# Kernel tuning notes

Measured on AMD Instinct MI355X. Metric: run time of the kernel, lower is better.

Reference implementation:

```python
import jax, jax.numpy as jnp
import numpy as np

B, T, IN, H, L, OUT, PRED, FN = 512, 96, 64, 512, 2, 1, 24, 32


def setup_inputs() -> dict:
    key = jax.random.key(0)
    ks = jax.random.split(key, 12)
    sc = 0.02
    n = lambda i, shape: jax.random.normal(ks[i], shape, jnp.float32) * sc
    return {
        "x": jax.random.normal(ks[0], (B, T, IN), jnp.float32),
        "station_id": jax.random.randint(ks[1], (B,), 0, 26, jnp.int32),
        "W_hidden": n(2, (H, IN)), "b_hidden": jnp.zeros((H,), jnp.float32),
        "embed": n(3, (26, H)),
        "W_ih": n(4, (L, 4 * H, H)), "W_hh": n(5, (L, 4 * H, H)),
        "b_ih": jnp.zeros((L, 4 * H), jnp.float32), "b_hh": jnp.zeros((L, 4 * H), jnp.float32),
        "conv_W": n(6, (FN, T - 1)), "conv_b": jnp.zeros((FN,), jnp.float32),
        "W1": n(7, (FN, H)), "b1": jnp.zeros((FN,), jnp.float32),
        "W2": n(8, (H, H + FN)), "b2": jnp.zeros((H,), jnp.float32),
        "W_out": n(9, (T * OUT, H)), "b_out": jnp.zeros((T * OUT,), jnp.float32),
    }


def _lstm(xc, W_ih, W_hh, b_ih, b_hh):
    # xc: [B, T, H]; multi-layer LSTM, PyTorch gate order i,f,g,o
    n_layers = W_ih.shape[0]
    h0 = jnp.zeros((n_layers, xc.shape[0], W_hh.shape[-1]), xc.dtype)

    def step(carry, xt):
        h, c = carry  # [L, B, H]
        inp = xt
        hs, cs = [], []
        for l in range(n_layers):
            g = inp @ W_ih[l].T + h[l] @ W_hh[l].T + b_ih[l] + b_hh[l]
            i, f, gg, o = jnp.split(g, 4, axis=-1)
            cn = jax.nn.sigmoid(f) * c[l] + jax.nn.sigmoid(i) * jnp.tanh(gg)
            hn = jax.nn.sigmoid(o) * jnp.tanh(cn)
            hs.append(hn); cs.append(cn)
            inp = hn
        return (jnp.stack(hs), jnp.stack(cs)), inp  # emit last-layer h

    _, outs = jax.lax.scan(step, (h0, h0), jnp.swapaxes(xc, 0, 1))
    return jnp.swapaxes(outs, 0, 1)  # [B, T, H] last-layer hidden states


def reference(x, station_id, W_hidden, b_hidden, embed, W_ih, W_hh, b_ih, b_hh,
              conv_W, conv_b, W1, b1, W2, b2, W_out, b_out):
    b, t, _ = x.shape
    hdim = W_hidden.shape[0]
    fn = conv_W.shape[0]
    xc = jax.nn.relu(x @ W_hidden.T + b_hidden)
    xc = xc + embed[station_id][:, None, :]
    hs_seq = _lstm(xc, W_ih, W_hh, b_ih, b_hh)          # [B, T, H]
    Hmat = jax.nn.relu(hs_seq[:, :-1, :])                # [B, T-1, H]
    htt = hs_seq[:, -1, :]                               # [B, H]
    # Conv2d(1, FN, (T-1, 1)) over [B,1,T-1,H] == contraction over time
    conv = jax.nn.relu(jnp.einsum('bth,ft->bfh', Hmat, conv_W) + conv_b[None, :, None])
    # original does .view(-1, feat_size, filter_num): raw reshape, not transpose
    feat = conv.reshape(b, hdim, fn)                     # [B, H, FN]
    w = (htt @ W1.T + b1)[:, None, :]                    # [B, 1, FN]
    alpha = jax.nn.sigmoid(jnp.sum(feat * w, axis=2))    # [B, H]
    v = jnp.sum(alpha[:, :, None] * feat, axis=1)        # [B, FN]
    new_ht = jnp.concatenate([htt, v], axis=1) @ W2.T + b2
    ypred = (new_ht @ W_out.T + b_out)[:, -PRED * OUT:]
    return ypred
```

## Files before the change

### kernel.cpp

```cpp
#include <hip/hip_runtime.h>
#include <math.h>

namespace {

constexpr int B = 512, T = 96, IN = 64, H = 512, G4 = 2048;
constexpr int FN = 32, KC = 544, NPRED = 24, TM1 = T - 1;
constexpr int BH = B * H;

typedef __attribute__((ext_vector_type(8))) short s8v;
typedef __attribute__((ext_vector_type(16))) float f16v;

__device__ __forceinline__ float sigf(float x) { return 1.0f / (1.0f + __expf(-x)); }
__device__ __forceinline__ float tanhfast(float x) {
  x = fminf(fmaxf(x, -15.f), 15.f);
  float e = __expf(2.0f * x);
  return (e - 1.0f) / (e + 1.0f);
}
__device__ __forceinline__ unsigned short bf16_rne(float f) {
  unsigned u = __float_as_uint(f);
  u += 0x7fffu + ((u >> 16) & 1u);
  return (unsigned short)(u >> 16);
}
__device__ __forceinline__ void split8(const float4& x, const float4& y, s8v& hi, s8v& lo) {
  float vs[8] = {x.x, x.y, x.z, x.w, y.x, y.y, y.z, y.w};
#pragma unroll
  for (int j = 0; j < 8; ++j) {
    unsigned ub = __float_as_uint(vs[j]);
    hi[j] = (short)(ub >> 16);
    lo[j] = (short)bf16_rne(vs[j] - __uint_as_float(ub & 0xffff0000u));
  }
}

__global__ __launch_bounds__(256) void k_xc(
    const float* __restrict__ x, const int* __restrict__ sid,
    const float* __restrict__ Wh, const float* __restrict__ bh,
    const float* __restrict__ emb, float* __restrict__ planes) {
  constexpr int RWS = 64;
  int row0 = blockIdx.x * RWS;
  int tid = threadIdx.x;
  __shared__ __align__(16) float sx[RWS][IN];
  {
    const float4* xsrc = (const float4*)(x + (size_t)row0 * IN);
    float4* sdst = (float4*)(&sx[0][0]);
    for (int i = tid; i < RWS * IN / 4; i += 256) sdst[i] = xsrc[i];
  }
  float4 w0[16], w1[16];
  const float* wr0 = Wh + (size_t)tid * IN;
  const float* wr1 = Wh + (size_t)(tid + 256) * IN;
#pragma unroll
  for (int j = 0; j < 16; ++j) {
    w0[j] = *(const float4*)(wr0 + j * 4);
    w1[j] = *(const float4*)(wr1 + j * 4);
  }
  float bb0 = bh[tid], bb1 = bh[tid + 256];
  __syncthreads();
#pragma unroll 2
  for (int r = 0; r < RWS; ++r) {
    float a00 = bb0, a01 = 0.f, a02 = 0.f, a03 = 0.f;
    float a10 = bb1, a11 = 0.f, a12 = 0.f, a13 = 0.f;
#pragma unroll
    for (int j = 0; j < 16; ++j) {
      float4 xv = *(const float4*)(&sx[r][j * 4]);
      a00 = fmaf(xv.x, w0[j].x, a00);
      a01 = fmaf(xv.y, w0[j].y, a01);
      a02 = fmaf(xv.z, w0[j].z, a02);
      a03 = fmaf(xv.w, w0[j].w, a03);
      a10 = fmaf(xv.x, w1[j].x, a10);
      a11 = fmaf(xv.y, w1[j].y, a11);
      a12 = fmaf(xv.z, w1[j].z, a12);
      a13 = fmaf(xv.w, w1[j].w, a13);
    }
    float acc0 = (a00 + a01) + (a02 + a03);
    float acc1 = (a10 + a11) + (a12 + a13);
    int row = row0 + r;
    int bb = row / T, t = row % T;
    const float* eb = emb + (size_t)sid[bb] * H;
    size_t o = ((size_t)t * B + bb) * H;
    planes[o + tid] = fmaxf(acc0, 0.f) + eb[tid];
    planes[o + tid + 256] = fmaxf(acc1, 0.f) + eb[tid + 256];
  }
}

__global__ __launch_bounds__(256) void k_wswz(
    const float* __restrict__ Wih, const float* __restrict__ Whh,
    short* __restrict__ WFhi, short* __restrict__ WFlo) {
  int g = blockIdx.x * 256 + threadIdx.x;
  int lane = g & 63;
  int fi = g >> 6;
  int nt = fi & 3, kt = (fi >> 2) & 63, ng = (fi >> 8) & 15, layer = fi >> 12;
  int row = nt * H + ng * 32 + (lane & 31);
  int kk = kt * 16 + (lane >> 5) * 8;
  const float* src = (kk < H) ? (Wih + ((size_t)layer * G4 + row) * H + kk)
                              : (Whh + ((size_t)layer * G4 + row) * H + (kk - H));
  float4 f0 = *(const float4*)src, f1 = *(const float4*)(src + 4);
  s8v hi, lo;
  split8(f0, f1, hi, lo);
  size_t o = (size_t)fi * 512 + lane * 8;
  *(s8v*)(WFhi + o) = hi;
  *(s8v*)(WFlo + o) = lo;
}

__global__ __launch_bounds__(256) void k_w2t(
    const float* __restrict__ W2, float* __restrict__ W2T4) {
  int g = blockIdx.x * 256 + threadIdx.x;
  int h = g / KC, k = g % KC;
  W2T4[((size_t)(k >> 2) * H + h) * 4 + (k & 3)] = W2[g];
}

__global__ __launch_bounds__(256, 1) void k_step(
    int tt, float* __restrict__ planes, const short* __restrict__ WFhi,
    const short* __restrict__ WFlo, short* __restrict__ hFhi,
    short* __restrict__ hFlo, const float* __restrict__ bih,
    const float* __restrict__ bhh, float* __restrict__ c0,
    float* __restrict__ c1) {
  int gid = blockIdx.x;
  int xcd = gid & 7;
  int u = gid >> 3;
  int combo = xcd * 4 + (u & 3);
  int layer = combo >> 4;
  if (layer ? (tt == 0) : (tt == T)) return;
  int ng = combo & 15;
  int b0 = (u >> 2) * 64;
  int step = layer ? (tt - 1) : tt;
  int tid = threadIdx.x, lane = tid & 63, wk = tid >> 6;
  int l31 = lane & 31, lh = lane >> 5;

  __shared__ float comb[4][4][32][32];

  const float* bi = bih + (size_t)layer * G4;
  const float* bh2 = bhh + (size_t)layer * G4;
  float* cbuf = layer ? c1 : c0;

  int rpar = (step - 1) & 1;
  const float* xbase = nullptr;
  const short *abhi = nullptr, *ablo = nullptr;
  if (layer == 0 && wk < 2) {
    xbase = planes + (size_t)step * BH + (size_t)(b0 + l31) * H + wk * 256 + lh * 8;
  } else {
    int src = (layer == 0) ? 0 : ((wk < 2) ? 0 : 1);
    int par = (layer == 0) ? rpar : ((wk < 2) ? (step & 1) : rpar);
    int kk0 = wk * 16 - ((layer == 0 || wk >= 2) ? 32 : 0);
    size_t o = ((((size_t)src * 2 + par) * 32 + kk0) * H + (b0 + l31)) * 16 + lh * 8;
    abhi = hFhi + o;
    ablo = hFlo + o;
  }

  float bias[4];
#pragma unroll
  for (int nt = 0; nt < 4; ++nt) {
    int r = nt * H + ng * 32 + l31;
    bias[nt] = bi[r] + bh2[r];
  }

  const size_t wstep = 4 * 512;
  const size_t wbase0 = ((size_t)(layer * 16 + ng) * 64 + wk * 16) * wstep + (size_t)lane * 8;
  const size_t astep = (size_t)H * 16;

  f16v acc[2][4];
#pragma unroll
  for (int rt = 0; rt < 2; ++rt)
#pragma unroll
    for (int nt = 0; nt < 4; ++nt)
#pragma unroll
      for (int e = 0; e < 16; ++e) acc[rt][nt][e] = 0.f;

  s8v a0h0, a0l0, a0h1, a0l1, b0h0, b0h1, b0h2, b0h3, b0l0, b0l1, b0l2, b0l3;
  s8v a1h0, a1l0, a1h1, a1l1, b1h0, b1h1, b1h2, b1h3, b1l0, b1l1, b1l2, b1l3;
  s8v a2h0, a2l0, a2h1, a2l1, b2h0, b2h1, b2h2, b2h3, b2l0, b2l1, b2l2, b2l3;

#define LOADW_(kq, bh0, bh1, bh2, bh3, bl0, bl1, bl2, bl3)          \
  {                                                                 \
    size_t wo = wbase0 + (size_t)(kq) * wstep;                      \
    bh0 = *(const s8v*)(WFhi + wo);                                 \
    bh1 = *(const s8v*)(WFhi + wo + 512);                           \
    bh2 = *(const s8v*)(WFhi + wo + 1024);                          \
    bh3 = *(const s8v*)(WFhi + wo + 1536);                          \
    bl0 = *(const s8v*)(WFlo + wo);                                 \
    bl1 = *(const s8v*)(WFlo + wo + 512);                           \
    bl2 = *(const s8v*)(WFlo + wo + 1024);                          \
    bl3 = *(const s8v*)(WFlo + wo + 1536);                          \
  }
#define LOADA_(kq, ah0, al0, ah1, al1)                              \
  {                                                                 \
    if (xbase) {                                                    \
      const float* ap = xbase + (kq) * 16;                          \
      float4 f0 = *(const float4*)ap, f1 = *(const float4*)(ap + 4);\
      split8(f0, f1, ah0, al0);                                     \
      const float* aq = ap + 32 * H;                                \
      float4 g0 = *(const float4*)aq, g1 = *(const float4*)(aq + 4);\
      split8(g0, g1, ah1, al1);                                     \
    } else {                                                        \
      const short* ph_ = abhi + (size_t)(kq) * astep;               \
      const short* pl_ = ablo + (size_t)(kq) * astep;               \
      ah0 = *(const s8v*)(ph_);                                     \
      al0 = *(const s8v*)(pl_);                                     \
      ah1 = *(const s8v*)(ph_ + 512);                               \
      al1 = *(const s8v*)(pl_ + 512);                               \
    }                                                               \
  }
#define MFMA3R_(rt, ah, al, bh0, bh1, bh2, bh3, bl0, bl1, bl2, bl3)                        \
  {                                                                                        \
    acc[rt][0] = __builtin_amdgcn_mfma_f32_32x32x16_bf16(ah, bh0, acc[rt][0], 0, 0, 0);    \
    acc[rt][1] = __builtin_amdgcn_mfma_f32_32x32x16_bf16(ah, bh1, acc[rt][1], 0, 0, 0);    \
    acc[rt][2] = __builtin_amdgcn_mfma_f32_32x32x16_bf16(ah, bh2, acc[rt][2], 0, 0, 0);    \
    acc[rt][3] = __builtin_amdgcn_mfma_f32_32x32x16_bf16(ah, bh3, acc[rt][3], 0, 0, 0);    \
    acc[rt][0] = __builtin_amdgcn_mfma_f32_32x32x16_bf16(ah, bl0, acc[rt][0], 0, 0, 0);    \
    acc[rt][1] = __builtin_amdgcn_mfma_f32_32x32x16_bf16(ah, bl1, acc[rt][1], 0, 0, 0);    \
    acc[rt][2] = __builtin_amdgcn_mfma_f32_32x32x16_bf16(ah, bl2, acc[rt][2], 0, 0, 0);    \
    acc[rt][3] = __builtin_amdgcn_mfma_f32_32x32x16_bf16(ah, bl3, acc[rt][3], 0, 0, 0);    \
    acc[rt][0] = __builtin_amdgcn_mfma_f32_32x32x16_bf16(al, bh0, acc[rt][0], 0, 0, 0);    \
    acc[rt][1] = __builtin_amdgcn_mfma_f32_32x32x16_bf16(al, bh1, acc[rt][1], 0, 0, 0);    \
    acc[rt][2] = __builtin_amdgcn_mfma_f32_32x32x16_bf16(al, bh2, acc[rt][2], 0, 0, 0);    \
    acc[rt][3] = __builtin_amdgcn_mfma_f32_32x32x16_bf16(al, bh3, acc[rt][3], 0, 0, 0);    \
  }
#define MFMA6_(ah0, al0, ah1, al1, bh0, bh1, bh2, bh3, bl0, bl1, bl2, bl3)  \
  {                                                                         \
    MFMA3R_(0, ah0, al0, bh0, bh1, bh2, bh3, bl0, bl1, bl2, bl3);           \
    MFMA3R_(1, ah1, al1, bh0, bh1, bh2, bh3, bl0, bl1, bl2, bl3);           \
  }

  LOADA_(0, a0h0, a0l0, a0h1, a0l1);
  LOADW_(0, b0h0, b0h1, b0h2, b0h3, b0l0, b0l1, b0l2, b0l3);
  LOADA_(1, a1h0, a1l0, a1h1, a1l1);
  LOADW_(1, b1h0, b1h1, b1h2, b1h3, b1l0, b1l1, b1l2, b1l3);
  LOADA_(2, a2h0, a2l0, a2h1, a2l1);
  LOADW_(2, b2h0, b2h1, b2h2, b2h3, b2l0, b2l1, b2l2, b2l3);
#pragma unroll 1
  for (int kp = 0; kp < 5; ++kp) {
    int kq = kp * 3;
    MFMA6_(a0h0, a0l0, a0h1, a0l1, b0h0, b0h1, b0h2, b0h3, b0l0, b0l1, b0l2, b0l3);
    LOADA_(kq + 3, a0h0, a0l0, a0h1, a0l1);
    LOADW_(kq + 3, b0h0, b0h1, b0h2, b0h3, b0l0, b0l1, b0l2, b0l3);
    MFMA6_(a1h0, a1l0, a1h1, a1l1, b1h0, b1h1, b1h2, b1h3, b1l0, b1l1, b1l2, b1l3);
    if (kp < 4) {
      LOADA_(kq + 4, a1h0, a1l0, a1h1, a1l1);
      LOADW_(kq + 4, b1h0, b1h1, b1h2, b1h3, b1l0, b1l1, b1l2, b1l3);
    }
    MFMA6_(a2h0, a2l0, a2h1, a2l1, b2h0, b2h1, b2h2, b2h3, b2l0, b2l1, b2l2, b2l3);
    if (kp < 4) {
      LOADA_(kq + 5, a2h0, a2l0, a2h1, a2l1);
      LOADW_(kq + 5, b2h0, b2h1, b2h2, b2h3, b2l0, b2l1, b2l2, b2l3);
    }
  }
  MFMA6_(a0h0, a0l0, a0h1, a0l1, b0h0, b0h1, b0h2, b0h3, b0l0, b0l1, b0l2, b0l3);
#undef LOADW_
#undef LOADA_
#undef MFMA3R_
#undef MFMA6_

#pragma unroll
  for (int rt = 0; rt < 2; ++rt) {
    if (rt) __syncthreads();
#pragma unroll
    for (int nt = 0; nt < 4; ++nt)
#pragma unroll
      for (int r = 0; r < 16; ++r) {
        int row = (r & 3) + 8 * (r >> 2) + 4 * lh;
        comb[nt][wk][row][l31] = acc[rt][nt][r];
      }
    __syncthreads();
    int b0p = b0 + rt * 32;
#pragma unroll
    for (int rr = 0; rr < 4; ++rr) {
      int r = wk * 4 + rr;
      int row = (r & 3) + 8 * (r >> 2) + 4 * lh;
      float g[4];
#pragma unroll
      for (int nt = 0; nt < 4; ++nt) {
        float p0 = comb[nt][0][row][l31];
        float p1 = comb[nt][1][row][l31];
        float p2 = comb[nt][2][row][l31];
        float p3 = comb[nt][3][row][l31];
        g[nt] = (p0 + p1) + (p2 + p3) + bias[nt];
      }
      size_t coff = (size_t)(b0p + row) * H + ng * 32 + l31;
      float cp = cbuf[coff];
      float cn = sigf(g[1]) * cp + sigf(g[0]) * tanhfast(g[2]);
      float hn = sigf(g[3]) * tanhfast(cn);
      cbuf[coff] = cn;
      int brow = b0p + row;
      int hcol = ng * 32 + l31;
      size_t o = ((((size_t)layer * 2 + (step & 1)) * 32 + (hcol >> 4)) * H + brow) * 16 + (hcol & 15);
      unsigned ub = __float_as_uint(hn);
      hFhi[o] = (short)(ub >> 16);
      hFlo[o] = (short)bf16_rne(hn - __uint_as_float(ub & 0xffff0000u));
      if (layer) planes[(size_t)step * BH + (size_t)brow * H + hcol] = hn;
    }
  }
}

__global__ __launch_bounds__(256) void k_conv(
    const float* __restrict__ hs, const float* __restrict__ cW,
    const float* __restrict__ cb, float* __restrict__ feat) {
  int b = blockIdx.x >> 2;
  int h0 = (blockIdx.x & 3) * 128;
  int tid = threadIdx.x;
  __shared__ float sW[TM1][FN];
  for (int i = tid; i < TM1 * FN; i += 256) sW[i >> 5][i & 31] = cW[(i & 31) * TM1 + (i >> 5)];
  __syncthreads();
  int hl = tid & 127, fg = (tid >> 7) * 16;
  float acc[16];
#pragma unroll
  for (int j = 0; j < 16; ++j) acc[j] = cb[fg + j];
  const float* hp = hs + (size_t)b * H + h0 + hl;
  for (int t = 0; t < TM1; ++t) {
    float v = fmaxf(hp[(size_t)t * BH], 0.f);
#pragma unroll
    for (int j = 0; j < 16; ++j) acc[j] = fmaf(v, sW[t][fg + j], acc[j]);
  }
#pragma unroll
  for (int j = 0; j < 16; ++j)
    feat[(size_t)b * (FN * H) + (size_t)(fg + j) * H + h0 + hl] = fmaxf(acc[j], 0.f);
}

__global__ __launch_bounds__(256) void k_attn(
    const float* __restrict__ hs, const float* __restrict__ feat,
    const float* __restrict__ W1, const float* __restrict__ b1,
    const float* __restrict__ W2T4, const float* __restrict__ b2,
    const float* __restrict__ Wout, const float* __restrict__ bout,
    float* __restrict__ out) {
  int b = blockIdx.x, tid = threadIdx.x;
  __shared__ __align__(16) float sh[H], snew[H], sw[FN], sv[FN];
  __shared__ __align__(16) float4 red4[32][8];
  const float* htt = hs + (size_t)(T - 1) * BH + (size_t)b * H;
  for (int i = tid; i < H; i += 256) sh[i] = htt[i];
  __syncthreads();
  {
    int f = tid >> 3, sl = tid & 7;
    const float* w1 = W1 + (size_t)f * H;
    float p = 0.f;
    for (int k = sl * 64; k < sl * 64 + 64; ++k) p = fmaf(sh[k], w1[k], p);
    p += __shfl_xor(p, 1); p += __shfl_xor(p, 2); p += __shfl_xor(p, 4);
    if (sl == 0) sw[f] = p + b1[f];
  }
  __syncthreads();
  const float* fb = feat + (size_t)b * (FN * H);
  int ig = tid >> 3, j0 = (tid & 7) * 4;
  float4 swv = *(const float4*)(&sw[j0]);
  float4 vacc = {0.f, 0.f, 0.f, 0.f};
#pragma unroll 4
  for (int p = 0; p < 16; ++p) {
    int i = p * 32 + ig;
    float4 f4 = *(const float4*)(fb + (size_t)i * FN + j0);
    float s = f4.x * swv.x;
    s = fmaf(f4.y, swv.y, s);
    s = fmaf(f4.z, swv.z, s);
    s = fmaf(f4.w, swv.w, s);
    s += __shfl_xor(s, 1); s += __shfl_xor(s, 2); s += __shfl_xor(s, 4);
    s = sigf(s);
    vacc.x = fmaf(s, f4.x, vacc.x);
    vacc.y = fmaf(s, f4.y, vacc.y);
    vacc.z = fmaf(s, f4.z, vacc.z);
    vacc.w = fmaf(s, f4.w, vacc.w);
  }
  red4[ig][tid & 7] = vacc;
  __syncthreads();
#pragma unroll
  for (int s2 = 16; s2 >= 1; s2 >>= 1) {
    if (tid < s2 * 8) {
      float4 a = red4[tid >> 3][tid & 7];
      float4 c = red4[(tid >> 3) + s2][tid & 7];
      a.x += c.x; a.y += c.y; a.z += c.z; a.w += c.w;
      red4[tid >> 3][tid & 7] = a;
    }
    __syncthreads();
  }
  if (tid < FN) sv[tid] = ((const float*)&red4[0][0])[tid];
  __syncthreads();
#pragma unroll
  for (int q = 0; q < 2; ++q) {
    int h = tid + q * 256;
    float p = b2[h];
    const float* wt = W2T4 + (size_t)h * 4;
#pragma unroll 4
    for (int kg = 0; kg < 128; ++kg) {
      float4 wv = *(const float4*)(wt + (size_t)kg * (H * 4));
      float4 shv = *(const float4*)(&sh[kg * 4]);
      p = fmaf(shv.x, wv.x, p);
      p = fmaf(shv.y, wv.y, p);
      p = fmaf(shv.z, wv.z, p);
      p = fmaf(shv.w, wv.w, p);
    }
#pragma unroll
    for (int kg = 128; kg < 136; ++kg) {
      float4 wv = *(const float4*)(wt + (size_t)kg * (H * 4));
      float4 svv = *(const float4*)(&sv[(kg - 128) * 4]);
      p = fmaf(svv.x, wv.x, p);
      p = fmaf(svv.y, wv.y, p);
      p = fmaf(svv.z, wv.z, p);
      p = fmaf(svv.w, wv.w, p);
    }
    snew[h] = p;
  }
  __syncthreads();
  if (tid < NPRED * 8) {
    int p = tid >> 3, sl = tid & 7;
    const float* wo = Wout + (size_t)(T - NPRED + p) * H;
    float sacc = 0.f;
    for (int k = sl * 64; k < sl * 64 + 64; ++k) sacc = fmaf(snew[k], wo[k], sacc);
    sacc += __shfl_xor(sacc, 1); sacc += __shfl_xor(sacc, 2); sacc += __shfl_xor(sacc, 4);
    if (sl == 0) out[(size_t)b * NPRED + p] = sacc + bout[T - NPRED + p];
  }
}

}

extern "C" void kernel_launch(void* const* d_in, const int* in_sizes, int n_in,
                              void* d_out, int out_size, void* d_ws, size_t ws_size,
                              hipStream_t stream) {
  const float* x    = (const float*)d_in[0];
  const int*   sid  = (const int*)d_in[1];
  const float* Wh   = (const float*)d_in[2];
  const float* bh   = (const float*)d_in[3];
  const float* emb  = (const float*)d_in[4];
  const float* Wih  = (const float*)d_in[5];
  const float* Whh  = (const float*)d_in[6];
  const float* bih  = (const float*)d_in[7];
  const float* bhh  = (const float*)d_in[8];
  const float* cW   = (const float*)d_in[9];
  const float* cb   = (const float*)d_in[10];
  const float* W1   = (const float*)d_in[11];
  const float* b1   = (const float*)d_in[12];
  const float* W2   = (const float*)d_in[13];
  const float* b2   = (const float*)d_in[14];
  const float* Wout = (const float*)d_in[15];
  const float* bout = (const float*)d_in[16];
  float* out = (float*)d_out;

  constexpr size_t HFE = (size_t)2 * 2 * 32 * H * 16;
  float* planes = (float*)d_ws;
  short* WFhi = (short*)(planes + (size_t)T * BH);
  short* WFlo = WFhi + (size_t)8192 * 512;
  short* hFhi = WFlo + (size_t)8192 * 512;
  short* hFlo = hFhi + HFE;
  float* cst = (float*)(hFlo + HFE);
  float* c0 = cst;
  float* c1 = cst + BH;
  float* feat = c1 + BH;
  float* w2t4 = feat + (size_t)B * FN * H;
  size_t need = (size_t)T * BH * 4 + (size_t)8192 * 512 * 2 * 2 + HFE * 2 * 2 +
                2 * (size_t)BH * 4 + (size_t)B * FN * H * 4 + (size_t)KC * H * 4;
  if (ws_size < need) return;

  hipMemsetAsync(hFhi, 0, HFE * 2 * 2 + 2 * (size_t)BH * 4, stream);
  k_xc<<<B * T / 64, 256, 0, stream>>>(x, sid, Wh, bh, emb, planes);
  k_wswz<<<2048, 256, 0, stream>>>(Wih, Whh, WFhi, WFlo);
  k_w2t<<<(H * KC) / 256, 256, 0, stream>>>(W2, w2t4);

  for (int tt = 0; tt <= T; ++tt)
    k_step<<<256, 256, 0, stream>>>(tt, planes, WFhi, WFlo, hFhi, hFlo, bih, bhh, c0, c1);

  k_conv<<<B * 4, 256, 0, stream>>>(planes, cW, cb, feat);
  k_attn<<<B, 256, 0, stream>>>(planes, feat, W1, b1, w2t4, b2, Wout, bout, out);
}
```

Baseline: 2.255 ms.

## Stage LSTM step weights through LDS with direct global-to-LDS loads

Weight fragments in the recurrent step kernel are now fetched with global_load_lds into a double-buffered shared-memory area and read back into registers just before the MFMAs. The previous triple-buffered register scheme is replaced by a two-deep LDS pipeline paced with explicit vmcnt waits and sched barriers. The aim is to cut VGPR pressure and to overlap weight fetch with the MFMA work. The vmcnt(12) accounting depends on the exact number of outstanding loads per stage, including the A-operand loads, so a miscount would read stale LDS data.

```diff
diff --git a/kernel.cpp b/kernel.cpp
--- a/kernel.cpp
+++ b/kernel.cpp
@@ -29,6 +29,11 @@
     hi[j] = (short)(ub >> 16);
     lo[j] = (short)bf16_rne(vs[j] - __uint_as_float(ub & 0xffff0000u));
   }
+}
+__device__ __forceinline__ void gll16(const short* g, short* l) {
+  __builtin_amdgcn_global_load_lds(
+      (__attribute__((address_space(1))) void*)(void*)g,
+      (__attribute__((address_space(3))) void*)l, 16, 0, 0);
 }
 
 __global__ __launch_bounds__(256) void k_xc(
@@ -125,6 +130,7 @@
   int tid = threadIdx.x, lane = tid & 63, wk = tid >> 6;
   int l31 = lane & 31, lh = lane >> 5;
 
+  __shared__ __align__(16) short sbw[4][2][8][512];
   __shared__ float comb[4][4][32][32];
 
   const float* bi = bih + (size_t)layer * G4;
@@ -151,6 +157,7 @@
     int r = nt * H + ng * 32 + l31;
     bias[nt] = bi[r] + bh2[r];
   }
+  asm volatile("s_waitcnt vmcnt(0)" ::: "memory");
 
   const size_t wstep = 4 * 512;
   const size_t wbase0 = ((size_t)(layer * 16 + ng) * 64 + wk * 16) * wstep + (size_t)lane * 8;
@@ -164,21 +171,34 @@
 #pragma unroll
       for (int e = 0; e < 16; ++e) acc[rt][nt][e] = 0.f;
 
-  s8v a0h0, a0l0, a0h1, a0l1, b0h0, b0h1, b0h2, b0h3, b0l0, b0l1, b0l2, b0l3;
-  s8v a1h0, a1l0, a1h1, a1l1, b1h0, b1h1, b1h2, b1h3, b1l0, b1l1, b1l2, b1l3;
-  s8v a2h0, a2l0, a2h1, a2l1, b2h0, b2h1, b2h2, b2h3, b2l0, b2l1, b2l2, b2l3;
-
-#define LOADW_(kq, bh0, bh1, bh2, bh3, bl0, bl1, bl2, bl3)          \
-  {                                                                 \
-    size_t wo = wbase0 + (size_t)(kq) * wstep;                      \
-    bh0 = *(const s8v*)(WFhi + wo);                                 \
-    bh1 = *(const s8v*)(WFhi + wo + 512);                           \
-    bh2 = *(const s8v*)(WFhi + wo + 1024);                          \
-    bh3 = *(const s8v*)(WFhi + wo + 1536);                          \
-    bl0 = *(const s8v*)(WFlo + wo);                                 \
-    bl1 = *(const s8v*)(WFlo + wo + 512);                           \
-    bl2 = *(const s8v*)(WFlo + wo + 1024);                          \
-    bl3 = *(const s8v*)(WFlo + wo + 1536);                          \
+  s8v a0h0, a0l0, a0h1, a0l1;
+  s8v a1h0, a1l0, a1h1, a1l1;
+  s8v wh0, wh1, wh2, wh3, wl0, wl1, wl2, wl3;
+
+#define STAGEW_(kq, b)                          \
+  {                                             \
+    size_t wo = wbase0 + (size_t)(kq) * wstep;  \
+    short* lb = &sbw[wk][b][0][0];              \
+    gll16(WFhi + wo, lb);                       \
+    gll16(WFhi + wo + 512, lb + 512);           \
+    gll16(WFhi + wo + 1024, lb + 1024);         \
+    gll16(WFhi + wo + 1536, lb + 1536);         \
+    gll16(WFlo + wo, lb + 2048);                \
+    gll16(WFlo + wo + 512, lb + 2560);          \
+    gll16(WFlo + wo + 1024, lb + 3072);         \
+    gll16(WFlo + wo + 1536, lb + 3584);         \
+  }
+#define LOADWS_(b)                                  \
+  {                                                 \
+    const short* lb = &sbw[wk][b][0][0] + lane * 8; \
+    wh0 = *(const s8v*)(lb);                        \
+    wh1 = *(const s8v*)(lb + 512);                  \
+    wh2 = *(const s8v*)(lb + 1024);                 \
+    wh3 = *(const s8v*)(lb + 1536);                 \
+    wl0 = *(const s8v*)(lb + 2048);                 \
+    wl1 = *(const s8v*)(lb + 2560);                 \
+    wl2 = *(const s8v*)(lb + 3072);                 \
+    wl3 = *(const s8v*)(lb + 3584);                 \
   }
 #define LOADA_(kq, ah0, al0, ah1, al1)                              \
   {                                                                 \
@@ -198,52 +218,58 @@
       al1 = *(const s8v*)(pl_ + 512);                               \
     }                                                               \
   }
-#define MFMA3R_(rt, ah, al, bh0, bh1, bh2, bh3, bl0, bl1, bl2, bl3)                        \
-  {                                                                                        \
-    acc[rt][0] = __builtin_amdgcn_mfma_f32_32x32x16_bf16(ah, bh0, acc[rt][0], 0, 0, 0);    \
-    acc[rt][1] = __builtin_amdgcn_mfma_f32_32x32x16_bf16(ah, bh1, acc[rt][1], 0, 0, 0);    \
-    acc[rt][2] = __builtin_amdgcn_mfma_f32_32x32x16_bf16(ah, bh2, acc[rt][2], 0, 0, 0);    \
-    acc[rt][3] = __builtin_amdgcn_mfma_f32_32x32x16_bf16(ah, bh3, acc[rt][3], 0, 0, 0);    \
-    acc[rt][0] = __builtin_amdgcn_mfma_f32_32x32x16_bf16(ah, bl0, acc[rt][0], 0, 0, 0);    \
-    acc[rt][1] = __builtin_amdgcn_mfma_f32_32x32x16_bf16(ah, bl1, acc[rt][1], 0, 0, 0);    \
-    acc[rt][2] = __builtin_amdgcn_mfma_f32_32x32x16_bf16(ah, bl2, acc[rt][2], 0, 0, 0);    \
-    acc[rt][3] = __builtin_amdgcn_mfma_f32_32x32x16_bf16(ah, bl3, acc[rt][3], 0, 0, 0);    \
-    acc[rt][0] = __builtin_amdgcn_mfma_f32_32x32x16_bf16(al, bh0, acc[rt][0], 0, 0, 0);    \
-    acc[rt][1] = __builtin_amdgcn_mfma_f32_32x32x16_bf16(al, bh1, acc[rt][1], 0, 0, 0);    \
-    acc[rt][2] = __builtin_amdgcn_mfma_f32_32x32x16_bf16(al, bh2, acc[rt][2], 0, 0, 0);    \
-    acc[rt][3] = __builtin_amdgcn_mfma_f32_32x32x16_bf16(al, bh3, acc[rt][3], 0, 0, 0);    \
-  }
-#define MFMA6_(ah0, al0, ah1, al1, bh0, bh1, bh2, bh3, bl0, bl1, bl2, bl3)  \
-  {                                                                         \
-    MFMA3R_(0, ah0, al0, bh0, bh1, bh2, bh3, bl0, bl1, bl2, bl3);           \
-    MFMA3R_(1, ah1, al1, bh0, bh1, bh2, bh3, bl0, bl1, bl2, bl3);           \
-  }
-
+#define MFMA3R_(rt, ah, al)                                                          \
+  {                                                                                  \
+    acc[rt][0] = __builtin_amdgcn_mfma_f32_32x32x16_bf16(ah, wh0, acc[rt][0], 0, 0, 0); \
+    acc[rt][1] = __builtin_amdgcn_mfma_f32_32x32x16_bf16(ah, wh1, acc[rt][1], 0, 0, 0); \
+    acc[rt][2] = __builtin_amdgcn_mfma_f32_32x32x16_bf16(ah, wh2, acc[rt][2], 0, 0, 0); \
+    acc[rt][3] = __builtin_amdgcn_mfma_f32_32x32x16_bf16(ah, wh3, acc[rt][3], 0, 0, 0); \
+    acc[rt][0] = __builtin_amdgcn_mfma_f32_32x32x16_bf16(ah, wl0, acc[rt][0], 0, 0, 0); \
+    acc[rt][1] = __builtin_amdgcn_mfma_f32_32x32x16_bf16(ah, wl1, acc[rt][1], 0, 0, 0); \
+    acc[rt][2] = __builtin_amdgcn_mfma_f32_32x32x16_bf16(ah, wl2, acc[rt][2], 0, 0, 0); \
+    acc[rt][3] = __builtin_amdgcn_mfma_f32_32x32x16_bf16(ah, wl3, acc[rt][3], 0, 0, 0); \
+    acc[rt][0] = __builtin_amdgcn_mfma_f32_32x32x16_bf16(al, wh0, acc[rt][0], 0, 0, 0); \
+    acc[rt][1] = __builtin_amdgcn_mfma_f32_32x32x16_bf16(al, wh1, acc[rt][1], 0, 0, 0); \
+    acc[rt][2] = __builtin_amdgcn_mfma_f32_32x32x16_bf16(al, wh2, acc[rt][2], 0, 0, 0); \
+    acc[rt][3] = __builtin_amdgcn_mfma_f32_32x32x16_bf16(al, wh3, acc[rt][3], 0, 0, 0); \
+  }
+#define MFMA6_(ah0, al0, ah1, al1) \
+  {                                \
+    MFMA3R_(0, ah0, al0);          \
+    MFMA3R_(1, ah1, al1);          \
+  }
+
+  STAGEW_(0, 0);
   LOADA_(0, a0h0, a0l0, a0h1, a0l1);
-  LOADW_(0, b0h0, b0h1, b0h2, b0h3, b0l0, b0l1, b0l2, b0l3);
+  STAGEW_(1, 1);
   LOADA_(1, a1h0, a1l0, a1h1, a1l1);
-  LOADW_(1, b1h0, b1h1, b1h2, b1h3, b1l0, b1l1, b1l2, b1l3);
-  LOADA_(2, a2h0, a2l0, a2h1, a2l1);
-  LOADW_(2, b2h0, b2h1, b2h2, b2h3, b2l0, b2l1, b2l2, b2l3);
+
 #pragma unroll 1
-  for (int kp = 0; kp < 5; ++kp) {
-    int kq = kp * 3;
-    MFMA6_(a0h0, a0l0, a0h1, a0l1, b0h0, b0h1, b0h2, b0h3, b0l0, b0l1, b0l2, b0l3);
-    LOADA_(kq + 3, a0h0, a0l0, a0h1, a0l1);
-    LOADW_(kq + 3, b0h0, b0h1, b0h2, b0h3, b0l0, b0l1, b0l2, b0l3);
-    MFMA6_(a1h0, a1l0, a1h1, a1l1, b1h0, b1h1, b1h2, b1h3, b1l0, b1l1, b1l2, b1l3);
-    if (kp < 4) {
-      LOADA_(kq + 4, a1h0, a1l0, a1h1, a1l1);
-      LOADW_(kq + 4, b1h0, b1h1, b1h2, b1h3, b1l0, b1l1, b1l2, b1l3);
-    }
-    MFMA6_(a2h0, a2l0, a2h1, a2l1, b2h0, b2h1, b2h2, b2h3, b2l0, b2l1, b2l2, b2l3);
-    if (kp < 4) {
-      LOADA_(kq + 5, a2h0, a2l0, a2h1, a2l1);
-      LOADW_(kq + 5, b2h0, b2h1, b2h2, b2h3, b2l0, b2l1, b2l2, b2l3);
-    }
-  }
-  MFMA6_(a0h0, a0l0, a0h1, a0l1, b0h0, b0h1, b0h2, b0h3, b0l0, b0l1, b0l2, b0l3);
-#undef LOADW_
+  for (int kp = 0; kp < 7; ++kp) {
+    int kq = kp * 2;
+    asm volatile("s_waitcnt vmcnt(12)" ::: "memory");
+    __builtin_amdgcn_sched_barrier(0);
+    LOADWS_(0);
+    MFMA6_(a0h0, a0l0, a0h1, a0l1);
+    STAGEW_(kq + 2, 0);
+    LOADA_(kq + 2, a0h0, a0l0, a0h1, a0l1);
+    asm volatile("s_waitcnt vmcnt(12)" ::: "memory");
+    __builtin_amdgcn_sched_barrier(0);
+    LOADWS_(1);
+    MFMA6_(a1h0, a1l0, a1h1, a1l1);
+    STAGEW_(kq + 3, 1);
+    LOADA_(kq + 3, a1h0, a1l0, a1h1, a1l1);
+  }
+  asm volatile("s_waitcnt vmcnt(12)" ::: "memory");
+  __builtin_amdgcn_sched_barrier(0);
+  LOADWS_(0);
+  MFMA6_(a0h0, a0l0, a0h1, a0l1);
+  asm volatile("s_waitcnt vmcnt(0)" ::: "memory");
+  __builtin_amdgcn_sched_barrier(0);
+  LOADWS_(1);
+  MFMA6_(a1h0, a1l0, a1h1, a1l1);
+#undef STAGEW_
+#undef LOADWS_
 #undef LOADA_
 #undef MFMA3R_
 #undef MFMA6_
```

Result: slower. 2.376 ms (+5.4%).
